# Performance work log

Hardware: AMD Instinct MI355X
Metric: run time of the kernel (lower is better)

Reference implementation:

```python
import jax, jax.numpy as jnp
import numpy as np


def setup_inputs() -> dict:
    key = jax.random.key(0)
    k1, k2 = jax.random.split(key)
    N, H, W, F = 32, 16, 16, 256
    B, C = 64, 8
    x = jax.random.normal(k1, (N, H, W, F), dtype=jnp.float32)
    # keras 'uniform' initializer: U(-0.05, 0.05)
    T = jax.random.uniform(k2, (F, B, C), dtype=jnp.float32, minval=-0.05, maxval=0.05)
    return {"x": x, "T": T}


def reference(x, T):
    # x: [N,H,W,F], T: [F,B,C]
    M = jnp.einsum('nhwf,fbc->nhwbc', x, T)            # [N,H,W,B,C]
    # all-pairs L1 distance over C between samples i and j
    diff = jnp.abs(M[:, None] - M[None, :])            # [N,N,H,W,B,C]
    norm = jnp.sum(diff, axis=-1)                      # [N,N,H,W,B]
    o_b = jnp.sum(jnp.exp(-norm), axis=1)              # [N,H,W,B]
    return jnp.concatenate([x, o_b], axis=3)           # [N,H,W,F+B]
```

## Files before the change

kernel.cpp:

```cpp
#include <hip/hip_runtime.h>
#include <hip/hip_bf16.h>


namespace {
constexpr int kN = 32;
constexpr int kHW = 256;
constexpr int kF = 256;
constexpr int kOutRow = 320;
constexpr int kMstride = 136;
constexpr int kOstride = 24;
}

using frag_ab = __attribute__((ext_vector_type(8))) short;
using frag_cd = __attribute__((ext_vector_type(4))) float;

__device__ inline unsigned short f2bf(float f) {
  union { __hip_bfloat16 h; unsigned short u; } c;
  c.h = __float2bfloat16(f);
  return c.u;
}

__device__ inline void unpack8(const uint4& m, float* f) {
  f[0] = __uint_as_float(m.x << 16);  f[1] = __uint_as_float(m.x & 0xffff0000u);
  f[2] = __uint_as_float(m.y << 16);  f[3] = __uint_as_float(m.y & 0xffff0000u);
  f[4] = __uint_as_float(m.z << 16);  f[5] = __uint_as_float(m.z & 0xffff0000u);
  f[6] = __uint_as_float(m.w << 16);  f[7] = __uint_as_float(m.w & 0xffff0000u);
}

__device__ inline uint4 pack_bf8(const float4& v0, const float4& v1) {
  uint4 p;
  p.x = (unsigned)f2bf(v0.x) | ((unsigned)f2bf(v0.y) << 16);
  p.y = (unsigned)f2bf(v0.z) | ((unsigned)f2bf(v0.w) << 16);
  p.z = (unsigned)f2bf(v1.x) | ((unsigned)f2bf(v1.y) << 16);
  p.w = (unsigned)f2bf(v1.z) | ((unsigned)f2bf(v1.w) << 16);
  return p;
}

__global__ __launch_bounds__(256)
void pack_T(const float* __restrict__ T, uint4* __restrict__ Tf) {
  const int g = blockIdx.x * 256 + threadIdx.x;
  const int l = g & 63;
  const int frag = g >> 6;
  const int tt = frag >> 3, kt = frag & 7;
  const int col = tt * 16 + (l & 15);
  const int k0 = kt * 32 + (l >> 4) * 8;
  unsigned p[4];
#pragma unroll
  for (int jj = 0; jj < 4; ++jj) {
    float a = T[(size_t)(k0 + jj * 2) * 512 + col];
    float b = T[(size_t)(k0 + jj * 2 + 1) * 512 + col];
    p[jj] = (unsigned)f2bf(a) | ((unsigned)f2bf(b) << 16);
  }
  Tf[g] = make_uint4(p[0], p[1], p[2], p[3]);
}

__global__ __launch_bounds__(256, 4)
void mbd_main(const float* __restrict__ x, const uint4* __restrict__ Tf,
              float* __restrict__ out) {
  __shared__ __align__(16) unsigned short Mlds[kN * kMstride];
  __shared__ float obuf[kN * kOstride];
  const int hw = blockIdx.x & (kHW - 1);
  const int qg = blockIdx.x >> 8;
  const int tid = threadIdx.x;
  const int l = tid & 63, w = tid >> 6;

  const float4* x4 = (const float4*)x;
  float4* out4 = (float4*)out;

  {
    const int n = tid >> 3;
    const int k8 = tid & 7;
    const size_t base = (size_t)(n * kHW + hw) * (kF / 4) + qg * 16 + k8 * 2;
    const size_t xb = (size_t)n * (kHW * kF / 4) + (size_t)hw * (kF / 4) +
                      qg * 16 + k8 * 2;
    float4 v0 = x4[xb];
    float4 v1 = x4[xb + 1];
    const size_t ob = (size_t)(n * kHW + hw) * (kOutRow / 4) + qg * 16 + k8 * 2;
    out4[ob] = v0;
    out4[ob + 1] = v1;
    (void)base;
  }

  frag_cd acc[2][2] = {};
  const size_t xrow0 = ((size_t)((l & 15) + 0) * kHW + hw) * kF + (l >> 4) * 8;
  const size_t xrow1 = ((size_t)((l & 15) + 16) * kHW + hw) * kF + (l >> 4) * 8;
#pragma unroll
  for (int kt = 0; kt < 8; ++kt) {
    float4 b00 = *(const float4*)&x[xrow0 + kt * 32];
    float4 b01 = *(const float4*)&x[xrow0 + kt * 32 + 4];
    float4 b10 = *(const float4*)&x[xrow1 + kt * 32];
    float4 b11 = *(const float4*)&x[xrow1 + kt * 32 + 4];
    uint4 bn0 = pack_bf8(b00, b01);
    uint4 bn1 = pack_bf8(b10, b11);
    frag_ab bf0 = __builtin_bit_cast(frag_ab, bn0);
    frag_ab bf1 = __builtin_bit_cast(frag_ab, bn1);
#pragma unroll
    for (int q = 0; q < 2; ++q) {
      const int tT = qg * 8 + w * 2 + q;
      uint4 a = Tf[(tT * 8 + kt) * 64 + l];
      frag_ab af = __builtin_bit_cast(frag_ab, a);
      acc[q][0] = __builtin_amdgcn_mfma_f32_16x16x32_bf16(af, bf0, acc[q][0], 0, 0, 0);
      acc[q][1] = __builtin_amdgcn_mfma_f32_16x16x32_bf16(af, bf1, acc[q][1], 0, 0, 0);
    }
  }

#pragma unroll
  for (int q = 0; q < 2; ++q)
#pragma unroll
    for (int nt = 0; nt < 2; ++nt)
#pragma unroll
      for (int r = 0; r < 4; ++r) {
        const int t = (w * 2 + q) * 16 + (l >> 4) * 4 + r;
        const int n = nt * 16 + (l & 15);
        Mlds[n * kMstride + t] = f2bf(acc[q][nt][r]);
      }
  __syncthreads();

  const int b = tid >> 4;
  const int i0 = (tid & 15) * 2;
  float mi[2][8];
#pragma unroll
  for (int ii = 0; ii < 2; ++ii) {
    uint4 m = *(const uint4*)&Mlds[(i0 + ii) * kMstride + b * 8];
    unpack8(m, mi[ii]);
  }
  float ob0 = 0.f, ob1 = 0.f;
#pragma unroll 4
  for (int j = 0; j < kN; ++j) {
    uint4 m = *(const uint4*)&Mlds[j * kMstride + b * 8];
    float mj[8];
    unpack8(m, mj);
    float n0 = 0.f, n1 = 0.f;
#pragma unroll
    for (int c = 0; c < 8; ++c) {
      n0 += fabsf(mi[0][c] - mj[c]);
      n1 += fabsf(mi[1][c] - mj[c]);
    }
    ob0 += __expf(-n0);
    ob1 += __expf(-n1);
  }
  obuf[i0 * kOstride + b] = ob0;
  obuf[(i0 + 1) * kOstride + b] = ob1;
  __syncthreads();

  if (tid < 128) {
    const int n = tid >> 2;
    const int b4 = tid & 3;
    float4 v = *(const float4*)&obuf[n * kOstride + b4 * 4];
    out4[(size_t)(n * kHW + hw) * (kOutRow / 4) + (kF / 4) + qg * 4 + b4] = v;
  }
}

extern "C" void kernel_launch(void* const* d_in, const int* in_sizes, int n_in,
                              void* d_out, int out_size, void* d_ws, size_t ws_size,
                              hipStream_t stream) {
  const float* x = (const float*)d_in[0];
  const float* T = (const float*)d_in[1];
  float* out = (float*)d_out;
  uint4* Tf = (uint4*)d_ws;
  (void)in_sizes; (void)n_in; (void)out_size; (void)ws_size;
  pack_T<<<dim3(64), dim3(256), 0, stream>>>(T, Tf);
  mbd_main<<<dim3(4 * kHW), dim3(256), 0, stream>>>(x, Tf, out);
}
```

Baseline: 85.60 us.

## Pre-pack x to bf16 fragments in prep kernel and halve per-block B work

A combined prep kernel copies x into the output and writes x as bf16 MFMA fragments to the workspace, alongside the T packing. The main kernel then reads packed bf16 fragments instead of re-reading and converting fp32 x, and the grid doubles to 8 groups per spatial position, each handling 8 B columns with one thread per (i,b) pair. The aim is to stop reloading fp32 x across the B groups and to raise parallelism. In exchange it adds a workspace round-trip of packed x (about 4 MB written and read) and doubles the number of blocks.

```diff
diff --git a/kernel.cpp b/kernel.cpp
--- a/kernel.cpp
+++ b/kernel.cpp
@@ -7,8 +7,9 @@
 constexpr int kHW = 256;
 constexpr int kF = 256;
 constexpr int kOutRow = 320;
-constexpr int kMstride = 136;
-constexpr int kOstride = 24;
+constexpr int kMstride = 72;
+constexpr int kOstride = 12;
+constexpr int kXfFrags = 1024;
 }
 
 using frag_ab = __attribute__((ext_vector_type(8))) short;
@@ -20,13 +21,6 @@
   return c.u;
 }
 
-__device__ inline void unpack8(const uint4& m, float* f) {
-  f[0] = __uint_as_float(m.x << 16);  f[1] = __uint_as_float(m.x & 0xffff0000u);
-  f[2] = __uint_as_float(m.y << 16);  f[3] = __uint_as_float(m.y & 0xffff0000u);
-  f[4] = __uint_as_float(m.z << 16);  f[5] = __uint_as_float(m.z & 0xffff0000u);
-  f[6] = __uint_as_float(m.w << 16);  f[7] = __uint_as_float(m.w & 0xffff0000u);
-}
-
 __device__ inline uint4 pack_bf8(const float4& v0, const float4& v1) {
   uint4 p;
   p.x = (unsigned)f2bf(v0.x) | ((unsigned)f2bf(v0.y) << 16);
@@ -36,118 +30,119 @@
   return p;
 }
 
+__device__ inline void unpack8(const uint4& m, float* f) {
+  f[0] = __uint_as_float(m.x << 16);  f[1] = __uint_as_float(m.x & 0xffff0000u);
+  f[2] = __uint_as_float(m.y << 16);  f[3] = __uint_as_float(m.y & 0xffff0000u);
+  f[4] = __uint_as_float(m.z << 16);  f[5] = __uint_as_float(m.z & 0xffff0000u);
+  f[6] = __uint_as_float(m.w << 16);  f[7] = __uint_as_float(m.w & 0xffff0000u);
+}
+
 __global__ __launch_bounds__(256)
-void pack_T(const float* __restrict__ T, uint4* __restrict__ Tf) {
-  const int g = blockIdx.x * 256 + threadIdx.x;
-  const int l = g & 63;
-  const int frag = g >> 6;
-  const int tt = frag >> 3, kt = frag & 7;
-  const int col = tt * 16 + (l & 15);
-  const int k0 = kt * 32 + (l >> 4) * 8;
-  unsigned p[4];
+void prep(const float* __restrict__ x, const float* __restrict__ T,
+          float* __restrict__ out, uint4* __restrict__ xf,
+          uint4* __restrict__ Tf) {
+  const int tid = threadIdx.x;
+  if (blockIdx.x < 256) {
+    const int hw = blockIdx.x;
+    const int l = tid & 63, w = tid >> 6;
 #pragma unroll
-  for (int jj = 0; jj < 4; ++jj) {
-    float a = T[(size_t)(k0 + jj * 2) * 512 + col];
-    float b = T[(size_t)(k0 + jj * 2 + 1) * 512 + col];
-    p[jj] = (unsigned)f2bf(a) | ((unsigned)f2bf(b) << 16);
+    for (int it = 0; it < 4; ++it) {
+      const int fg = it * 4 + w;
+      const int rt = fg >> 3, kt = fg & 7;
+      const int n = rt * 16 + (l & 15);
+      const int k0 = kt * 32 + (l >> 4) * 8;
+      const float* xp = x + ((size_t)(n * kHW + hw) * kF + k0);
+      float4 v0 = *(const float4*)xp;
+      float4 v1 = *(const float4*)(xp + 4);
+      float* op = out + ((size_t)(n * kHW + hw) * kOutRow + k0);
+      *(float4*)op = v0;
+      *(float4*)(op + 4) = v1;
+      xf[(size_t)hw * kXfFrags + fg * 64 + l] = pack_bf8(v0, v1);
+    }
+  } else {
+    const int g = (blockIdx.x - 256) * 256 + tid;
+    const int l = g & 63;
+    const int frag = g >> 6;
+    const int tt = frag >> 3, kt = frag & 7;
+    const int col = tt * 16 + (l & 15);
+    const int k0 = kt * 32 + (l >> 4) * 8;
+    unsigned p[4];
+#pragma unroll
+    for (int jj = 0; jj < 4; ++jj) {
+      float a = T[(size_t)(k0 + jj * 2) * 512 + col];
+      float b = T[(size_t)(k0 + jj * 2 + 1) * 512 + col];
+      p[jj] = (unsigned)f2bf(a) | ((unsigned)f2bf(b) << 16);
+    }
+    Tf[g] = make_uint4(p[0], p[1], p[2], p[3]);
   }
-  Tf[g] = make_uint4(p[0], p[1], p[2], p[3]);
 }
 
 __global__ __launch_bounds__(256, 4)
-void mbd_main(const float* __restrict__ x, const uint4* __restrict__ Tf,
+void mbd_main(const uint4* __restrict__ xf, const uint4* __restrict__ Tf,
               float* __restrict__ out) {
   __shared__ __align__(16) unsigned short Mlds[kN * kMstride];
   __shared__ float obuf[kN * kOstride];
   const int hw = blockIdx.x & (kHW - 1);
-  const int qg = blockIdx.x >> 8;
+  const int g = blockIdx.x >> 8;
   const int tid = threadIdx.x;
   const int l = tid & 63, w = tid >> 6;
+  const int tT = g * 4 + w;
 
-  const float4* x4 = (const float4*)x;
-  float4* out4 = (float4*)out;
+  uint4 Bf[8], Af[2][8];
+#pragma unroll
+  for (int kt = 0; kt < 8; ++kt) Bf[kt] = Tf[(tT * 8 + kt) * 64 + l];
+#pragma unroll
+  for (int rt = 0; rt < 2; ++rt)
+#pragma unroll
+    for (int kt = 0; kt < 8; ++kt)
+      Af[rt][kt] = xf[(size_t)hw * kXfFrags + (rt * 8 + kt) * 64 + l];
 
-  {
-    const int n = tid >> 3;
-    const int k8 = tid & 7;
-    const size_t base = (size_t)(n * kHW + hw) * (kF / 4) + qg * 16 + k8 * 2;
-    const size_t xb = (size_t)n * (kHW * kF / 4) + (size_t)hw * (kF / 4) +
-                      qg * 16 + k8 * 2;
-    float4 v0 = x4[xb];
-    float4 v1 = x4[xb + 1];
-    const size_t ob = (size_t)(n * kHW + hw) * (kOutRow / 4) + qg * 16 + k8 * 2;
-    out4[ob] = v0;
-    out4[ob + 1] = v1;
-    (void)base;
-  }
-
-  frag_cd acc[2][2] = {};
-  const size_t xrow0 = ((size_t)((l & 15) + 0) * kHW + hw) * kF + (l >> 4) * 8;
-  const size_t xrow1 = ((size_t)((l & 15) + 16) * kHW + hw) * kF + (l >> 4) * 8;
+  frag_cd acc[2] = {};
 #pragma unroll
   for (int kt = 0; kt < 8; ++kt) {
-    float4 b00 = *(const float4*)&x[xrow0 + kt * 32];
-    float4 b01 = *(const float4*)&x[xrow0 + kt * 32 + 4];
-    float4 b10 = *(const float4*)&x[xrow1 + kt * 32];
-    float4 b11 = *(const float4*)&x[xrow1 + kt * 32 + 4];
-    uint4 bn0 = pack_bf8(b00, b01);
-    uint4 bn1 = pack_bf8(b10, b11);
-    frag_ab bf0 = __builtin_bit_cast(frag_ab, bn0);
-    frag_ab bf1 = __builtin_bit_cast(frag_ab, bn1);
-#pragma unroll
-    for (int q = 0; q < 2; ++q) {
-      const int tT = qg * 8 + w * 2 + q;
-      uint4 a = Tf[(tT * 8 + kt) * 64 + l];
-      frag_ab af = __builtin_bit_cast(frag_ab, a);
-      acc[q][0] = __builtin_amdgcn_mfma_f32_16x16x32_bf16(af, bf0, acc[q][0], 0, 0, 0);
-      acc[q][1] = __builtin_amdgcn_mfma_f32_16x16x32_bf16(af, bf1, acc[q][1], 0, 0, 0);
-    }
+    frag_ab bf = __builtin_bit_cast(frag_ab, Bf[kt]);
+    acc[0] = __builtin_amdgcn_mfma_f32_16x16x32_bf16(
+        __builtin_bit_cast(frag_ab, Af[0][kt]), bf, acc[0], 0, 0, 0);
+    acc[1] = __builtin_amdgcn_mfma_f32_16x16x32_bf16(
+        __builtin_bit_cast(frag_ab, Af[1][kt]), bf, acc[1], 0, 0, 0);
   }
 
 #pragma unroll
-  for (int q = 0; q < 2; ++q)
+  for (int rt = 0; rt < 2; ++rt)
 #pragma unroll
-    for (int nt = 0; nt < 2; ++nt)
-#pragma unroll
-      for (int r = 0; r < 4; ++r) {
-        const int t = (w * 2 + q) * 16 + (l >> 4) * 4 + r;
-        const int n = nt * 16 + (l & 15);
-        Mlds[n * kMstride + t] = f2bf(acc[q][nt][r]);
-      }
+    for (int r = 0; r < 4; ++r) {
+      const int n = rt * 16 + (l >> 4) * 4 + r;
+      const int t = w * 16 + (l & 15);
+      Mlds[n * kMstride + t] = f2bf(acc[rt][r]);
+    }
   __syncthreads();
 
-  const int b = tid >> 4;
-  const int i0 = (tid & 15) * 2;
-  float mi[2][8];
-#pragma unroll
-  for (int ii = 0; ii < 2; ++ii) {
-    uint4 m = *(const uint4*)&Mlds[(i0 + ii) * kMstride + b * 8];
-    unpack8(m, mi[ii]);
+  const int b = tid >> 5;
+  const int i = tid & 31;
+  float mi[8];
+  {
+    uint4 m = *(const uint4*)&Mlds[i * kMstride + b * 8];
+    unpack8(m, mi);
   }
-  float ob0 = 0.f, ob1 = 0.f;
-#pragma unroll 4
+  float ob = 0.f;
+#pragma unroll 8
   for (int j = 0; j < kN; ++j) {
     uint4 m = *(const uint4*)&Mlds[j * kMstride + b * 8];
     float mj[8];
     unpack8(m, mj);
-    float n0 = 0.f, n1 = 0.f;
+    float nrm = 0.f;
 #pragma unroll
-    for (int c = 0; c < 8; ++c) {
-      n0 += fabsf(mi[0][c] - mj[c]);
-      n1 += fabsf(mi[1][c] - mj[c]);
-    }
-    ob0 += __expf(-n0);
-    ob1 += __expf(-n1);
+    for (int c = 0; c < 8; ++c) nrm += fabsf(mi[c] - mj[c]);
+    ob += __expf(-nrm);
   }
-  obuf[i0 * kOstride + b] = ob0;
-  obuf[(i0 + 1) * kOstride + b] = ob1;
+  obuf[i * kOstride + b] = ob;
   __syncthreads();
 
-  if (tid < 128) {
-    const int n = tid >> 2;
-    const int b4 = tid & 3;
+  if (tid < 64) {
+    const int n = tid >> 1;
+    const int b4 = tid & 1;
     float4 v = *(const float4*)&obuf[n * kOstride + b4 * 4];
-    out4[(size_t)(n * kHW + hw) * (kOutRow / 4) + (kF / 4) + qg * 4 + b4] = v;
+    *(float4*)&out[(size_t)(n * kHW + hw) * kOutRow + kF + g * 8 + b4 * 4] = v;
   }
 }
 
@@ -157,8 +152,9 @@
   const float* x = (const float*)d_in[0];
   const float* T = (const float*)d_in[1];
   float* out = (float*)d_out;
-  uint4* Tf = (uint4*)d_ws;
+  uint4* xf = (uint4*)d_ws;
+  uint4* Tf = (uint4*)d_ws + (size_t)kHW * kXfFrags;
   (void)in_sizes; (void)n_in; (void)out_size; (void)ws_size;
-  pack_T<<<dim3(64), dim3(256), 0, stream>>>(T, Tf);
-  mbd_main<<<dim3(4 * kHW), dim3(256), 0, stream>>>(x, Tf, out);
+  prep<<<dim3(320), dim3(256), 0, stream>>>(x, T, out, xf, Tf);
+  mbd_main<<<dim3(8 * kHW), dim3(256), 0, stream>>>(xf, Tf, out);
 }
```

Measured after the change: 79.36 us. 1.08x faster.
